# Performance work log

Hardware: AMD Instinct MI355X
Metric: run time of the kernel (lower is better)

The kernel has to match this reference:

```python
import jax, jax.numpy as jnp
import numpy as np

B, T, C = 4, 4096, 1024
HEAD = 128


def setup_inputs() -> dict:
    key = jax.random.key(0)
    k0, k1, k2, k3 = jax.random.split(key, 4)
    x = jax.random.normal(k0, (B, T, C), dtype=jnp.float32)
    # bias-free linear weights, stored as (in, out) so y = x @ W
    Wk = jax.random.normal(k1, (C, HEAD), dtype=jnp.float32) * (C ** -0.5)
    Wq = jax.random.normal(k2, (C, HEAD), dtype=jnp.float32) * (C ** -0.5)
    Wv = jax.random.normal(k3, (C, HEAD), dtype=jnp.float32) * (C ** -0.5)
    return {"x": x, "Wk": Wk, "Wq": Wq, "Wv": Wv}


def reference(x, Wk, Wq, Wv):
    Bx, Tx, Cx = x.shape
    k = x @ Wk            # [B,T,H]
    q = x @ Wq            # [B,T,H]
    v = x @ Wv            # [B,T,H]
    # NOTE: original code scales by C**-0.5 where C = n_embd (input dim), not head_size
    scale = Cx ** -0.5
    wei = jnp.einsum("bqh,bkh->bqk", q, k) * scale        # [B,T,T]
    causal = jnp.arange(Tx)[:, None] >= jnp.arange(Tx)[None, :]
    wei = jnp.where(causal, wei, -jnp.inf)
    wei = jax.nn.softmax(wei, axis=-1)
    # dropout rate is 0.0 in the source -> identity
    return jnp.einsum("bqk,bkh->bqh", wei, v)             # [B,T,H]
```

## Files before the change

kernel.cpp:

```cpp
#include <hip/hip_runtime.h>


typedef __bf16 bf16;
typedef bf16 bf16x8 __attribute__((ext_vector_type(8)));
typedef bf16 bf16x4 __attribute__((ext_vector_type(4)));
typedef float f32x4 __attribute__((ext_vector_type(4)));

#define L2E 1.4426950408889634f
#define TSEQ 4096
#define CDIM 1024
#define HDIM 128
#define MROWS 16384

#define GLDS(g, l)                                              \
  __builtin_amdgcn_global_load_lds(                             \
      (__attribute__((address_space(1))) void*)(g),             \
      (__attribute__((address_space(3))) void*)(l), 16, 0, 0)

static __device__ inline unsigned pkbf(float a, float b) {
  union { bf16 h; unsigned short u; } ua, ub;
  ua.h = (bf16)a; ub.h = (bf16)b;
  return ((unsigned)ub.u << 16) | (unsigned)ua.u;
}

__global__ __launch_bounds__(256) void wt_prep(const float* __restrict__ Wq,
                                               const float* __restrict__ Wk,
                                               const float* __restrict__ Wv,
                                               bf16* __restrict__ WT) {
  const int mode = blockIdx.y;
  const float* W = (mode == 0) ? Wq : (mode == 1) ? Wk : Wv;
  const int idx = blockIdx.x * 256 + threadIdx.x;
  const int n = idx >> 10;
  const int k = idx & 1023;
  WT[(size_t)mode * 131072 + idx] = (bf16)W[(size_t)k * HDIM + n];
}

__global__ __launch_bounds__(256) void qkv_gemm(const float* __restrict__ x,
                                                const bf16* __restrict__ WT,
                                                bf16* __restrict__ qb,
                                                bf16* __restrict__ kb,
                                                bf16* __restrict__ vT) {
  __shared__ __attribute__((aligned(16))) bf16 a_tile[128 * 32];
  __shared__ __attribute__((aligned(16))) bf16 b_tile[128 * 32];
  const int tid = threadIdx.x;
  const int wid = tid >> 6;
  const int lane = tid & 63;
  const int lr = lane & 15;
  const int lg = lane >> 4;
  const int wr = wid >> 1;
  const int wc = wid & 1;
  const int mode = blockIdx.y;
  const int m0 = blockIdx.x * 128;
  const bf16* wt = WT + (size_t)mode * 131072;

  int rowA[2], col8[2];
#pragma unroll
  for (int g = 0; g < 2; ++g) {
    const int idx8 = g * 256 + tid;
    rowA[g] = idx8 >> 2;
    col8[g] = (idx8 & 3) * 8;
  }

  f32x4 acc[4][4] = {};

  float4 fA[2][2];
  bf16x8 fB[2];
#pragma unroll
  for (int g = 0; g < 2; ++g) {
    const float* src = x + (size_t)(m0 + rowA[g]) * CDIM + col8[g];
    fA[g][0] = *(const float4*)src;
    fA[g][1] = *(const float4*)(src + 4);
    fB[g] = *(const bf16x8*)(wt + (size_t)rowA[g] * CDIM + col8[g]);
  }

#pragma unroll 1
  for (int kt = 0; kt < 32; ++kt) {
    __syncthreads();
#pragma unroll
    for (int g = 0; g < 2; ++g) {
      bf16x8 av;
      av[0] = (bf16)fA[g][0].x; av[1] = (bf16)fA[g][0].y;
      av[2] = (bf16)fA[g][0].z; av[3] = (bf16)fA[g][0].w;
      av[4] = (bf16)fA[g][1].x; av[5] = (bf16)fA[g][1].y;
      av[6] = (bf16)fA[g][1].z; av[7] = (bf16)fA[g][1].w;
      *(bf16x8*)&a_tile[rowA[g] * 32 + col8[g]] = av;
      *(bf16x8*)&b_tile[rowA[g] * 32 + col8[g]] = fB[g];
    }
    __syncthreads();
    if (kt + 1 < 32) {
#pragma unroll
      for (int g = 0; g < 2; ++g) {
        const float* src = x + (size_t)(m0 + rowA[g]) * CDIM + (kt + 1) * 32 + col8[g];
        fA[g][0] = *(const float4*)src;
        fA[g][1] = *(const float4*)(src + 4);
        fB[g] = *(const bf16x8*)(wt + (size_t)rowA[g] * CDIM + (kt + 1) * 32 + col8[g]);
      }
    }
    bf16x8 af[4], bfr[4];
#pragma unroll
    for (int r = 0; r < 4; ++r)
      af[r] = *(const bf16x8*)&a_tile[(wr * 64 + r * 16 + lr) * 32 + lg * 8];
#pragma unroll
    for (int c = 0; c < 4; ++c)
      bfr[c] = *(const bf16x8*)&b_tile[(wc * 64 + c * 16 + lr) * 32 + lg * 8];
#pragma unroll
    for (int r = 0; r < 4; ++r)
#pragma unroll
      for (int c = 0; c < 4; ++c)
        acc[r][c] = __builtin_amdgcn_mfma_f32_16x16x32_bf16(af[r], bfr[c], acc[r][c], 0, 0, 0);
  }

  if (mode < 2) {
    bf16* dst = (mode == 0) ? qb : kb;
    const float sc = (mode == 0) ? 0.03125f : 1.0f;
#pragma unroll
    for (int r = 0; r < 4; ++r)
#pragma unroll
      for (int c = 0; c < 4; ++c)
#pragma unroll
        for (int j = 0; j < 4; ++j) {
          const int row = m0 + wr * 64 + r * 16 + lg * 4 + j;
          const int col = wc * 64 + c * 16 + lr;
          dst[(size_t)row * HDIM + col] = (bf16)(acc[r][c][j] * sc);
        }
  } else {
#pragma unroll
    for (int r = 0; r < 4; ++r)
#pragma unroll
      for (int c = 0; c < 4; ++c) {
        const int row0 = m0 + wr * 64 + r * 16 + lg * 4;
        const int col = wc * 64 + c * 16 + lr;
        bf16x4 pv;
        pv[0] = (bf16)acc[r][c][0]; pv[1] = (bf16)acc[r][c][1];
        pv[2] = (bf16)acc[r][c][2]; pv[3] = (bf16)acc[r][c][3];
        *(bf16x4*)(vT + (size_t)col * MROWS + row0) = pv;
      }
  }
}

__global__ __launch_bounds__(256) void attn_part(const bf16* __restrict__ qb,
                                                 const bf16* __restrict__ kb,
                                                 const bf16* __restrict__ vT,
                                                 bf16* __restrict__ po,
                                                 float* __restrict__ pm,
                                                 float* __restrict__ pl,
                                                 int cshift, int maxc) {
  __shared__ __attribute__((aligned(16))) char kv_lds[2][32768];
  __shared__ __attribute__((aligned(16))) bf16 p_lds[4][16][72];
  const int tid = threadIdx.x;
  const int wid = tid >> 6;
  const int lane = tid & 63;
  const int lr = lane & 15;
  const int lg = lane >> 4;
  const int b = blockIdx.z;
  const int c = blockIdx.y;
  const int qbase = blockIdx.x * 64;
  const int kv0 = c << cshift;
  if (kv0 >= qbase + 64) return;
  const int kvend = min(kv0 + (1 << cshift), qbase + 64);
  const int nt = (kvend - kv0) >> 6;
  const int qr0 = qbase + wid * 16;
  const int grp = blockIdx.x * 4 + wid;
  const size_t qrow = (size_t)b * TSEQ + qr0;

  const int wbase = wid * 4096;
  int ksrc[4], vsrc[4];
#pragma unroll
  for (int i = 0; i < 4; ++i) {
    const int o = wbase + i * 1024 + lane * 16;
    const int rk = o >> 8;
    ksrc[i] = rk * 256 + ((o & 255) ^ ((rk & 7) << 4));
    const int rv = o >> 7;
    vsrc[i] = rv * (MROWS * 2) + ((o & 127) ^ ((rv & 7) << 4));
  }
  const char* kgb = (const char*)kb + (size_t)b * TSEQ * 256;
  const char* vgb = (const char*)vT + (size_t)b * TSEQ * 2;

  const int m30 = (lr & 3) << 4;
  const int m6 = (lr & 4) << 4;
  const int lgx = (lg * 16) ^ m30;
  const int kreadA = lr * 256 + lgx + m6;
  const int kreadB = lr * 256 + lgx + (64 ^ m6);
  const int vreadA = 16384 + lr * 128 + lgx + m6;
  const int vreadB = 16384 + lr * 128 + lgx + (64 ^ m6);

  bf16x8 qf[4];
#pragma unroll
  for (int d = 0; d < 4; ++d)
    qf[d] = *(const bf16x8*)(qb + (qrow + lr) * HDIM + d * 32 + lg * 8);

  f32x4 o_[8] = {};
  float m_ = -1e30f, l_ = 0.0f;

  {
    const char* ks = kgb + (size_t)kv0 * 256;
    const char* vs = vgb + (size_t)kv0 * 2;
#pragma unroll
    for (int i = 0; i < 4; ++i) {
      GLDS(ks + ksrc[i], &kv_lds[0][wbase + i * 1024]);
      GLDS(vs + vsrc[i], &kv_lds[0][16384 + wbase + i * 1024]);
    }
  }
  __syncthreads();

  int cur = 0;
  for (int t = 0; t < nt; ++t) {
    const int kvt = kv0 + (t << 6);
    if (t + 1 < nt) {
      const char* ks = kgb + (size_t)(kvt + 64) * 256;
      const char* vs = vgb + (size_t)(kvt + 64) * 2;
#pragma unroll
      for (int i = 0; i < 4; ++i) {
        GLDS(ks + ksrc[i], &kv_lds[cur ^ 1][wbase + i * 1024]);
        GLDS(vs + vsrc[i], &kv_lds[cur ^ 1][16384 + wbase + i * 1024]);
      }
    }
    if (kvt < qr0 + 16) {
      const char* kbuf = kv_lds[cur];
      f32x4 s[4] = {};
      __builtin_amdgcn_s_setprio(1);
#pragma unroll
      for (int nf = 0; nf < 4; ++nf) {
        const char* kb0 = kbuf + nf * 4096;
        bf16x8 kf;
        kf = *(const bf16x8*)(kb0 + kreadA);
        s[nf] = __builtin_amdgcn_mfma_f32_16x16x32_bf16(kf, qf[0], s[nf], 0, 0, 0);
        kf = *(const bf16x8*)(kb0 + kreadB);
        s[nf] = __builtin_amdgcn_mfma_f32_16x16x32_bf16(kf, qf[1], s[nf], 0, 0, 0);
        kf = *(const bf16x8*)(kb0 + kreadA + 128);
        s[nf] = __builtin_amdgcn_mfma_f32_16x16x32_bf16(kf, qf[2], s[nf], 0, 0, 0);
        kf = *(const bf16x8*)(kb0 + kreadB + 128);
        s[nf] = __builtin_amdgcn_mfma_f32_16x16x32_bf16(kf, qf[3], s[nf], 0, 0, 0);
      }
      __builtin_amdgcn_s_setprio(0);
      if (kvt + 63 >= qr0) {
        const int q = qr0 + lr;
#pragma unroll
        for (int nf = 0; nf < 4; ++nf)
#pragma unroll
          for (int j = 0; j < 4; ++j)
            if (kvt + nf * 16 + lg * 4 + j > q) s[nf][j] = -1e30f;
      }
      float rmax = fmaxf(fmaxf(s[0][0], s[0][1]), fmaxf(s[0][2], s[0][3]));
#pragma unroll
      for (int nf = 1; nf < 4; ++nf)
        rmax = fmaxf(rmax, fmaxf(fmaxf(s[nf][0], s[nf][1]), fmaxf(s[nf][2], s[nf][3])));
      rmax = fmaxf(rmax, __shfl_xor(rmax, 16));
      rmax = fmaxf(rmax, __shfl_xor(rmax, 32));
      const float mn = fmaxf(m_, rmax);
      const float al = exp2f((m_ - mn) * L2E);
      m_ = mn;
      float rsum = 0.0f;
#pragma unroll
      for (int nf = 0; nf < 4; ++nf)
#pragma unroll
        for (int j = 0; j < 4; ++j) {
          s[nf][j] = exp2f((s[nf][j] - mn) * L2E);
          rsum += s[nf][j];
        }
      rsum += __shfl_xor(rsum, 16);
      rsum += __shfl_xor(rsum, 32);
      l_ = l_ * al + rsum;
#pragma unroll
      for (int o = 0; o < 8; ++o)
#pragma unroll
        for (int j = 0; j < 4; ++j)
          o_[o][j] *= al;
      {
        unsigned* pw = (unsigned*)&p_lds[wid][0][0];
        const int base = lr * 36 + lg * 2;
#pragma unroll
        for (int nf = 0; nf < 4; ++nf) {
          pw[base + nf * 8]     = pkbf(s[nf][0], s[nf][1]);
          pw[base + nf * 8 + 1] = pkbf(s[nf][2], s[nf][3]);
        }
      }
      asm volatile("s_waitcnt lgkmcnt(0)" ::: "memory");
      __builtin_amdgcn_sched_barrier(0);
      bf16x8 pf0 = *(const bf16x8*)&p_lds[wid][lr][lg * 8];
      bf16x8 pf1 = *(const bf16x8*)&p_lds[wid][lr][32 + lg * 8];
      __builtin_amdgcn_s_setprio(1);
#pragma unroll
      for (int o = 0; o < 8; ++o) {
        bf16x8 vf;
        vf = *(const bf16x8*)(kbuf + vreadA + o * 2048);
        o_[o] = __builtin_amdgcn_mfma_f32_16x16x32_bf16(vf, pf0, o_[o], 0, 0, 0);
        vf = *(const bf16x8*)(kbuf + vreadB + o * 2048);
        o_[o] = __builtin_amdgcn_mfma_f32_16x16x32_bf16(vf, pf1, o_[o], 0, 0, 0);
      }
      __builtin_amdgcn_s_setprio(0);
    }
    __syncthreads();
    cur ^= 1;
  }

  const size_t slot = (size_t)(b * 256 + grp) * maxc + c;
  bf16* pob = po + slot * (16 * HDIM);
#pragma unroll
  for (int o = 0; o < 8; ++o) {
    bf16x4 pv;
    pv[0] = (bf16)o_[o][0]; pv[1] = (bf16)o_[o][1];
    pv[2] = (bf16)o_[o][2]; pv[3] = (bf16)o_[o][3];
    *(bf16x4*)(pob + lr * HDIM + o * 16 + lg * 4) = pv;
  }
  if (lg == 0) {
    pm[slot * 16 + lr] = m_;
    pl[slot * 16 + lr] = l_;
  }
}

__global__ __launch_bounds__(256) void attn_merge(const bf16* __restrict__ po,
                                                  const float* __restrict__ pm,
                                                  const float* __restrict__ pl,
                                                  float* __restrict__ out,
                                                  int cshift, int maxc) {
  const int bg = blockIdx.x;
  const int g = bg & 255;
  const int nch = ((g << 4) >> cshift) + 1;
  const int row = threadIdx.x >> 4;
  const int d8 = (threadIdx.x & 15) * 8;
  const size_t slot0 = (size_t)bg * maxc;

  float M = -1e30f;
  for (int c = 0; c < nch; ++c) M = fmaxf(M, pm[(slot0 + c) * 16 + row]);
  float L = 0.0f;
  float acc[8] = {};
  for (int c = 0; c < nch; ++c) {
    const float w = exp2f((pm[(slot0 + c) * 16 + row] - M) * L2E);
    L += w * pl[(slot0 + c) * 16 + row];
    const bf16x8 v = *(const bf16x8*)(po + (slot0 + c) * (16 * HDIM) + row * HDIM + d8);
#pragma unroll
    for (int i = 0; i < 8; ++i) acc[i] += w * (float)v[i];
  }
  const float inv = 1.0f / L;
  f32x4 r0, r1;
#pragma unroll
  for (int i = 0; i < 4; ++i) { r0[i] = acc[i] * inv; r1[i] = acc[i + 4] * inv; }
  float* dst = out + (size_t)bg * (16 * HDIM) + row * HDIM + d8;
  *(f32x4*)dst = r0;
  *(f32x4*)(dst + 4) = r1;
}

extern "C" void kernel_launch(void* const* d_in, const int* in_sizes, int n_in,
                              void* d_out, int out_size, void* d_ws, size_t ws_size,
                              hipStream_t stream) {
  const float* x  = (const float*)d_in[0];
  const float* Wk = (const float*)d_in[1];
  const float* Wq = (const float*)d_in[2];
  const float* Wv = (const float*)d_in[3];
  float* out = (float*)d_out;

  char* ws = (char*)d_ws;
  bf16* qb = (bf16*)(ws);
  bf16* kb = (bf16*)(ws + 4194304);
  bf16* vT = (bf16*)(ws + 8388608);
  bf16* WT = (bf16*)(ws + 12582912);
  const size_t pbase = 13369344;

  int cshift, maxc;
  if (ws_size >= pbase + 8ull * 1024 * 4224) { cshift = 9;  maxc = 8; }
  else if (ws_size >= pbase + 4ull * 1024 * 4224) { cshift = 10; maxc = 4; }
  else { cshift = 12; maxc = 1; }
  bf16* po = (bf16*)(ws + pbase);
  float* pm = (float*)(ws + pbase + (size_t)maxc * 1024 * 16 * 128 * 2);
  float* pl = pm + (size_t)maxc * 1024 * 16;

  wt_prep<<<dim3(512, 3), 256, 0, stream>>>(Wq, Wk, Wv, WT);
  qkv_gemm<<<dim3(128, 3), 256, 0, stream>>>(x, WT, qb, kb, vT);
  attn_part<<<dim3(64, maxc, 4), 256, 0, stream>>>(qb, kb, vT, po, pm, pl, cshift, maxc);
  attn_merge<<<1024, 256, 0, stream>>>(po, pm, pl, out, cshift, maxc);
}
```

Measured before the change: 103.6 us.

## Process 32 query rows per wave and skip small max rescales in attention

After: 101.5 us. 2.0% less time.

```diff
diff --git a/kernel.cpp b/kernel.cpp
--- a/kernel.cpp
+++ b/kernel.cpp
@@ -138,15 +138,15 @@
   }
 }
 
-__global__ __launch_bounds__(256) void attn_part(const bf16* __restrict__ qb,
-                                                 const bf16* __restrict__ kb,
-                                                 const bf16* __restrict__ vT,
-                                                 bf16* __restrict__ po,
-                                                 float* __restrict__ pm,
-                                                 float* __restrict__ pl,
-                                                 int cshift, int maxc) {
+__global__ __launch_bounds__(256, 2) void attn_part(const bf16* __restrict__ qg,
+                                                    const bf16* __restrict__ kb,
+                                                    const bf16* __restrict__ vT,
+                                                    bf16* __restrict__ po,
+                                                    float* __restrict__ pm,
+                                                    float* __restrict__ pl,
+                                                    int cshift, int maxc) {
   __shared__ __attribute__((aligned(16))) char kv_lds[2][32768];
-  __shared__ __attribute__((aligned(16))) bf16 p_lds[4][16][72];
+  __shared__ __attribute__((aligned(16))) bf16 p_lds[4][32][64];
   const int tid = threadIdx.x;
   const int wid = tid >> 6;
   const int lane = tid & 63;
@@ -154,14 +154,14 @@
   const int lg = lane >> 4;
   const int b = blockIdx.z;
   const int c = blockIdx.y;
-  const int qbase = blockIdx.x * 64;
+  const int qbase = blockIdx.x * 128;
   const int kv0 = c << cshift;
-  if (kv0 >= qbase + 64) return;
-  const int kvend = min(kv0 + (1 << cshift), qbase + 64);
+  if (kv0 >= qbase + 128) return;
+  const int kvend = min(kv0 + (1 << cshift), qbase + 128);
   const int nt = (kvend - kv0) >> 6;
-  const int qr0 = qbase + wid * 16;
-  const int grp = blockIdx.x * 4 + wid;
-  const size_t qrow = (size_t)b * TSEQ + qr0;
+  const int qr0w = qbase + wid * 32;
+  const int grp0 = blockIdx.x * 8 + wid * 2;
+  const size_t qrow = (size_t)b * TSEQ + qr0w;
 
   const int wbase = wid * 4096;
   int ksrc[4], vsrc[4];
@@ -176,6 +176,7 @@
   const char* kgb = (const char*)kb + (size_t)b * TSEQ * 256;
   const char* vgb = (const char*)vT + (size_t)b * TSEQ * 2;
 
+  const int msk = (lr & 7) << 4;
   const int m30 = (lr & 3) << 4;
   const int m6 = (lr & 4) << 4;
   const int lgx = (lg * 16) ^ m30;
@@ -184,13 +185,16 @@
   const int vreadA = 16384 + lr * 128 + lgx + m6;
   const int vreadB = 16384 + lr * 128 + lgx + (64 ^ m6);
 
-  bf16x8 qf[4];
-#pragma unroll
-  for (int d = 0; d < 4; ++d)
-    qf[d] = *(const bf16x8*)(qb + (qrow + lr) * HDIM + d * 32 + lg * 8);
-
-  f32x4 o_[8] = {};
-  float m_ = -1e30f, l_ = 0.0f;
+  bf16x8 qa[4], qc[4];
+#pragma unroll
+  for (int d = 0; d < 4; ++d) {
+    qa[d] = *(const bf16x8*)(qg + (qrow + lr) * HDIM + d * 32 + lg * 8);
+    qc[d] = *(const bf16x8*)(qg + (qrow + 16 + lr) * HDIM + d * 32 + lg * 8);
+  }
+
+  f32x4 o0_[8] = {}, o1_[8] = {};
+  float m0_ = -1e30f, l0_ = 0.0f;
+  float m1_ = -1e30f, l1_ = 0.0f;
 
   {
     const char* ks = kgb + (size_t)kv0 * 256;
@@ -215,78 +219,98 @@
         GLDS(vs + vsrc[i], &kv_lds[cur ^ 1][16384 + wbase + i * 1024]);
       }
     }
-    if (kvt < qr0 + 16) {
+    if (kvt < qr0w + 32) {
       const char* kbuf = kv_lds[cur];
-      f32x4 s[4] = {};
+      f32x4 s0[4] = {}, s1[4] = {};
       __builtin_amdgcn_s_setprio(1);
 #pragma unroll
       for (int nf = 0; nf < 4; ++nf) {
         const char* kb0 = kbuf + nf * 4096;
         bf16x8 kf;
         kf = *(const bf16x8*)(kb0 + kreadA);
-        s[nf] = __builtin_amdgcn_mfma_f32_16x16x32_bf16(kf, qf[0], s[nf], 0, 0, 0);
+        s0[nf] = __builtin_amdgcn_mfma_f32_16x16x32_bf16(kf, qa[0], s0[nf], 0, 0, 0);
+        s1[nf] = __builtin_amdgcn_mfma_f32_16x16x32_bf16(kf, qc[0], s1[nf], 0, 0, 0);
         kf = *(const bf16x8*)(kb0 + kreadB);
-        s[nf] = __builtin_amdgcn_mfma_f32_16x16x32_bf16(kf, qf[1], s[nf], 0, 0, 0);
+        s0[nf] = __builtin_amdgcn_mfma_f32_16x16x32_bf16(kf, qa[1], s0[nf], 0, 0, 0);
+        s1[nf] = __builtin_amdgcn_mfma_f32_16x16x32_bf16(kf, qc[1], s1[nf], 0, 0, 0);
         kf = *(const bf16x8*)(kb0 + kreadA + 128);
-        s[nf] = __builtin_amdgcn_mfma_f32_16x16x32_bf16(kf, qf[2], s[nf], 0, 0, 0);
+        s0[nf] = __builtin_amdgcn_mfma_f32_16x16x32_bf16(kf, qa[2], s0[nf], 0, 0, 0);
+        s1[nf] = __builtin_amdgcn_mfma_f32_16x16x32_bf16(kf, qc[2], s1[nf], 0, 0, 0);
         kf = *(const bf16x8*)(kb0 + kreadB + 128);
-        s[nf] = __builtin_amdgcn_mfma_f32_16x16x32_bf16(kf, qf[3], s[nf], 0, 0, 0);
+        s0[nf] = __builtin_amdgcn_mfma_f32_16x16x32_bf16(kf, qa[3], s0[nf], 0, 0, 0);
+        s1[nf] = __builtin_amdgcn_mfma_f32_16x16x32_bf16(kf, qc[3], s1[nf], 0, 0, 0);
       }
       __builtin_amdgcn_s_setprio(0);
-      if (kvt + 63 >= qr0) {
-        const int q = qr0 + lr;
+      if (kvt + 63 >= qr0w) {
+        const int q0 = qr0w + lr;
+        const int q1 = q0 + 16;
 #pragma unroll
         for (int nf = 0; nf < 4; ++nf)
 #pragma unroll
-          for (int j = 0; j < 4; ++j)
-            if (kvt + nf * 16 + lg * 4 + j > q) s[nf][j] = -1e30f;
-      }
-      float rmax = fmaxf(fmaxf(s[0][0], s[0][1]), fmaxf(s[0][2], s[0][3]));
-#pragma unroll
-      for (int nf = 1; nf < 4; ++nf)
-        rmax = fmaxf(rmax, fmaxf(fmaxf(s[nf][0], s[nf][1]), fmaxf(s[nf][2], s[nf][3])));
-      rmax = fmaxf(rmax, __shfl_xor(rmax, 16));
-      rmax = fmaxf(rmax, __shfl_xor(rmax, 32));
-      const float mn = fmaxf(m_, rmax);
-      const float al = exp2f((m_ - mn) * L2E);
-      m_ = mn;
-      float rsum = 0.0f;
+          for (int j = 0; j < 4; ++j) {
+            const int key = kvt + nf * 16 + lg * 4 + j;
+            if (key > q0) s0[nf][j] = -1e30f;
+            if (key > q1) s1[nf][j] = -1e30f;
+          }
+      }
+      float r0 = fmaxf(fmaxf(s0[0][0], s0[0][1]), fmaxf(s0[0][2], s0[0][3]));
+      float r1 = fmaxf(fmaxf(s1[0][0], s1[0][1]), fmaxf(s1[0][2], s1[0][3]));
+#pragma unroll
+      for (int nf = 1; nf < 4; ++nf) {
+        r0 = fmaxf(r0, fmaxf(fmaxf(s0[nf][0], s0[nf][1]), fmaxf(s0[nf][2], s0[nf][3])));
+        r1 = fmaxf(r1, fmaxf(fmaxf(s1[nf][0], s1[nf][1]), fmaxf(s1[nf][2], s1[nf][3])));
+      }
+      r0 = fmaxf(r0, __shfl_xor(r0, 16)); r0 = fmaxf(r0, __shfl_xor(r0, 32));
+      r1 = fmaxf(r1, __shfl_xor(r1, 16)); r1 = fmaxf(r1, __shfl_xor(r1, 32));
+      if (!__all(r0 <= m0_ + 8.0f && r1 <= m1_ + 8.0f)) {
+        const float mn0 = fmaxf(m0_, r0), mn1 = fmaxf(m1_, r1);
+        const float al0 = exp2f((m0_ - mn0) * L2E);
+        const float al1 = exp2f((m1_ - mn1) * L2E);
+        m0_ = mn0; m1_ = mn1;
+        l0_ *= al0; l1_ *= al1;
+#pragma unroll
+        for (int o = 0; o < 8; ++o)
+#pragma unroll
+          for (int j = 0; j < 4; ++j) { o0_[o][j] *= al0; o1_[o][j] *= al1; }
+      }
+      float rs0 = 0.0f, rs1 = 0.0f;
 #pragma unroll
       for (int nf = 0; nf < 4; ++nf)
 #pragma unroll
         for (int j = 0; j < 4; ++j) {
-          s[nf][j] = exp2f((s[nf][j] - mn) * L2E);
-          rsum += s[nf][j];
+          s0[nf][j] = exp2f((s0[nf][j] - m0_) * L2E); rs0 += s0[nf][j];
+          s1[nf][j] = exp2f((s1[nf][j] - m1_) * L2E); rs1 += s1[nf][j];
         }
-      rsum += __shfl_xor(rsum, 16);
-      rsum += __shfl_xor(rsum, 32);
-      l_ = l_ * al + rsum;
-#pragma unroll
-      for (int o = 0; o < 8; ++o)
-#pragma unroll
-        for (int j = 0; j < 4; ++j)
-          o_[o][j] *= al;
       {
-        unsigned* pw = (unsigned*)&p_lds[wid][0][0];
-        const int base = lr * 36 + lg * 2;
+        char* pw = (char*)p_lds + wid * 4096 + lr * 128;
 #pragma unroll
         for (int nf = 0; nf < 4; ++nf) {
-          pw[base + nf * 8]     = pkbf(s[nf][0], s[nf][1]);
-          pw[base + nf * 8 + 1] = pkbf(s[nf][2], s[nf][3]);
+          uint2 w2;
+          w2.x = pkbf(s0[nf][0], s0[nf][1]); w2.y = pkbf(s0[nf][2], s0[nf][3]);
+          *(uint2*)(pw + (((nf * 32) + lg * 8) ^ msk)) = w2;
+          w2.x = pkbf(s1[nf][0], s1[nf][1]); w2.y = pkbf(s1[nf][2], s1[nf][3]);
+          *(uint2*)(pw + 2048 + (((nf * 32) + lg * 8) ^ msk)) = w2;
         }
       }
+      rs0 += __shfl_xor(rs0, 16); rs0 += __shfl_xor(rs0, 32); l0_ += rs0;
+      rs1 += __shfl_xor(rs1, 16); rs1 += __shfl_xor(rs1, 32); l1_ += rs1;
       asm volatile("s_waitcnt lgkmcnt(0)" ::: "memory");
       __builtin_amdgcn_sched_barrier(0);
-      bf16x8 pf0 = *(const bf16x8*)&p_lds[wid][lr][lg * 8];
-      bf16x8 pf1 = *(const bf16x8*)&p_lds[wid][lr][32 + lg * 8];
+      const char* pr = (const char*)p_lds + wid * 4096 + lr * 128;
+      bf16x8 p00 = *(const bf16x8*)(pr + lgx + m6);
+      bf16x8 p01 = *(const bf16x8*)(pr + lgx + (64 ^ m6));
+      bf16x8 p10 = *(const bf16x8*)(pr + 2048 + lgx + m6);
+      bf16x8 p11 = *(const bf16x8*)(pr + 2048 + lgx + (64 ^ m6));
       __builtin_amdgcn_s_setprio(1);
 #pragma unroll
       for (int o = 0; o < 8; ++o) {
         bf16x8 vf;
         vf = *(const bf16x8*)(kbuf + vreadA + o * 2048);
-        o_[o] = __builtin_amdgcn_mfma_f32_16x16x32_bf16(vf, pf0, o_[o], 0, 0, 0);
+        o0_[o] = __builtin_amdgcn_mfma_f32_16x16x32_bf16(vf, p00, o0_[o], 0, 0, 0);
+        o1_[o] = __builtin_amdgcn_mfma_f32_16x16x32_bf16(vf, p10, o1_[o], 0, 0, 0);
         vf = *(const bf16x8*)(kbuf + vreadB + o * 2048);
-        o_[o] = __builtin_amdgcn_mfma_f32_16x16x32_bf16(vf, pf1, o_[o], 0, 0, 0);
+        o0_[o] = __builtin_amdgcn_mfma_f32_16x16x32_bf16(vf, p01, o0_[o], 0, 0, 0);
+        o1_[o] = __builtin_amdgcn_mfma_f32_16x16x32_bf16(vf, p11, o1_[o], 0, 0, 0);
       }
       __builtin_amdgcn_s_setprio(0);
     }
@@ -294,18 +318,23 @@
     cur ^= 1;
   }
 
-  const size_t slot = (size_t)(b * 256 + grp) * maxc + c;
-  bf16* pob = po + slot * (16 * HDIM);
+  const size_t slot0 = (size_t)(b * 256 + grp0) * maxc + c;
+  const size_t slot1 = slot0 + maxc;
+  bf16* pob0 = po + slot0 * (16 * HDIM);
+  bf16* pob1 = po + slot1 * (16 * HDIM);
 #pragma unroll
   for (int o = 0; o < 8; ++o) {
     bf16x4 pv;
-    pv[0] = (bf16)o_[o][0]; pv[1] = (bf16)o_[o][1];
-    pv[2] = (bf16)o_[o][2]; pv[3] = (bf16)o_[o][3];
-    *(bf16x4*)(pob + lr * HDIM + o * 16 + lg * 4) = pv;
+    pv[0] = (bf16)o0_[o][0]; pv[1] = (bf16)o0_[o][1];
+    pv[2] = (bf16)o0_[o][2]; pv[3] = (bf16)o0_[o][3];
+    *(bf16x4*)(pob0 + lr * HDIM + o * 16 + lg * 4) = pv;
+    pv[0] = (bf16)o1_[o][0]; pv[1] = (bf16)o1_[o][1];
+    pv[2] = (bf16)o1_[o][2]; pv[3] = (bf16)o1_[o][3];
+    *(bf16x4*)(pob1 + lr * HDIM + o * 16 + lg * 4) = pv;
   }
   if (lg == 0) {
-    pm[slot * 16 + lr] = m_;
-    pl[slot * 16 + lr] = l_;
+    pm[slot0 * 16 + lr] = m0_; pl[slot0 * 16 + lr] = l0_;
+    pm[slot1 * 16 + lr] = m1_; pl[slot1 * 16 + lr] = l1_;
   }
 }
 
@@ -367,6 +396,6 @@
 
   wt_prep<<<dim3(512, 3), 256, 0, stream>>>(Wq, Wk, Wv, WT);
   qkv_gemm<<<dim3(128, 3), 256, 0, stream>>>(x, WT, qb, kb, vT);
-  attn_part<<<dim3(64, maxc, 4), 256, 0, stream>>>(qb, kb, vT, po, pm, pl, cshift, maxc);
+  attn_part<<<dim3(32, maxc, 4), 256, 0, stream>>>(qb, kb, vT, po, pm, pl, cshift, maxc);
   attn_merge<<<1024, 256, 0, stream>>>(po, pm, pl, out, cshift, maxc);
 }
```

## Widen attention blocks to 8 waves, add lazy rescale and swizzled P tile

Applied to the files above, without the earlier changes.

Result: faster. 100.7 us (-2.8%).

```diff
diff --git a/kernel.cpp b/kernel.cpp
--- a/kernel.cpp
+++ b/kernel.cpp
@@ -138,15 +138,15 @@
   }
 }
 
-__global__ __launch_bounds__(256) void attn_part(const bf16* __restrict__ qb,
-                                                 const bf16* __restrict__ kb,
-                                                 const bf16* __restrict__ vT,
-                                                 bf16* __restrict__ po,
-                                                 float* __restrict__ pm,
-                                                 float* __restrict__ pl,
-                                                 int cshift, int maxc) {
+__global__ __launch_bounds__(512, 4) void attn_part(const bf16* __restrict__ qg,
+                                                    const bf16* __restrict__ kb,
+                                                    const bf16* __restrict__ vT,
+                                                    bf16* __restrict__ po,
+                                                    float* __restrict__ pm,
+                                                    float* __restrict__ pl,
+                                                    int cshift, int maxc) {
   __shared__ __attribute__((aligned(16))) char kv_lds[2][32768];
-  __shared__ __attribute__((aligned(16))) bf16 p_lds[4][16][72];
+  __shared__ __attribute__((aligned(16))) bf16 p_lds[8][16][64];
   const int tid = threadIdx.x;
   const int wid = tid >> 6;
   const int lane = tid & 63;
@@ -154,19 +154,19 @@
   const int lg = lane >> 4;
   const int b = blockIdx.z;
   const int c = blockIdx.y;
-  const int qbase = blockIdx.x * 64;
+  const int qbase = blockIdx.x * 128;
   const int kv0 = c << cshift;
-  if (kv0 >= qbase + 64) return;
-  const int kvend = min(kv0 + (1 << cshift), qbase + 64);
+  if (kv0 >= qbase + 128) return;
+  const int kvend = min(kv0 + (1 << cshift), qbase + 128);
   const int nt = (kvend - kv0) >> 6;
   const int qr0 = qbase + wid * 16;
-  const int grp = blockIdx.x * 4 + wid;
+  const int grp = blockIdx.x * 8 + wid;
   const size_t qrow = (size_t)b * TSEQ + qr0;
 
-  const int wbase = wid * 4096;
-  int ksrc[4], vsrc[4];
-#pragma unroll
-  for (int i = 0; i < 4; ++i) {
+  const int wbase = wid * 2048;
+  int ksrc[2], vsrc[2];
+#pragma unroll
+  for (int i = 0; i < 2; ++i) {
     const int o = wbase + i * 1024 + lane * 16;
     const int rk = o >> 8;
     ksrc[i] = rk * 256 + ((o & 255) ^ ((rk & 7) << 4));
@@ -176,6 +176,7 @@
   const char* kgb = (const char*)kb + (size_t)b * TSEQ * 256;
   const char* vgb = (const char*)vT + (size_t)b * TSEQ * 2;
 
+  const int msk = (lr & 7) << 4;
   const int m30 = (lr & 3) << 4;
   const int m6 = (lr & 4) << 4;
   const int lgx = (lg * 16) ^ m30;
@@ -187,7 +188,7 @@
   bf16x8 qf[4];
 #pragma unroll
   for (int d = 0; d < 4; ++d)
-    qf[d] = *(const bf16x8*)(qb + (qrow + lr) * HDIM + d * 32 + lg * 8);
+    qf[d] = *(const bf16x8*)(qg + (qrow + lr) * HDIM + d * 32 + lg * 8);
 
   f32x4 o_[8] = {};
   float m_ = -1e30f, l_ = 0.0f;
@@ -196,7 +197,7 @@
     const char* ks = kgb + (size_t)kv0 * 256;
     const char* vs = vgb + (size_t)kv0 * 2;
 #pragma unroll
-    for (int i = 0; i < 4; ++i) {
+    for (int i = 0; i < 2; ++i) {
       GLDS(ks + ksrc[i], &kv_lds[0][wbase + i * 1024]);
       GLDS(vs + vsrc[i], &kv_lds[0][16384 + wbase + i * 1024]);
     }
@@ -210,7 +211,7 @@
       const char* ks = kgb + (size_t)(kvt + 64) * 256;
       const char* vs = vgb + (size_t)(kvt + 64) * 2;
 #pragma unroll
-      for (int i = 0; i < 4; ++i) {
+      for (int i = 0; i < 2; ++i) {
         GLDS(ks + ksrc[i], &kv_lds[cur ^ 1][wbase + i * 1024]);
         GLDS(vs + vsrc[i], &kv_lds[cur ^ 1][16384 + wbase + i * 1024]);
       }
@@ -247,38 +248,39 @@
         rmax = fmaxf(rmax, fmaxf(fmaxf(s[nf][0], s[nf][1]), fmaxf(s[nf][2], s[nf][3])));
       rmax = fmaxf(rmax, __shfl_xor(rmax, 16));
       rmax = fmaxf(rmax, __shfl_xor(rmax, 32));
-      const float mn = fmaxf(m_, rmax);
-      const float al = exp2f((m_ - mn) * L2E);
-      m_ = mn;
+      if (!__all(rmax <= m_ + 8.0f)) {
+        const float mn = fmaxf(m_, rmax);
+        const float al = exp2f((m_ - mn) * L2E);
+        m_ = mn;
+        l_ *= al;
+#pragma unroll
+        for (int o = 0; o < 8; ++o)
+#pragma unroll
+          for (int j = 0; j < 4; ++j) o_[o][j] *= al;
+      }
       float rsum = 0.0f;
 #pragma unroll
       for (int nf = 0; nf < 4; ++nf)
 #pragma unroll
         for (int j = 0; j < 4; ++j) {
-          s[nf][j] = exp2f((s[nf][j] - mn) * L2E);
+          s[nf][j] = exp2f((s[nf][j] - m_) * L2E);
           rsum += s[nf][j];
         }
-      rsum += __shfl_xor(rsum, 16);
-      rsum += __shfl_xor(rsum, 32);
-      l_ = l_ * al + rsum;
-#pragma unroll
-      for (int o = 0; o < 8; ++o)
-#pragma unroll
-        for (int j = 0; j < 4; ++j)
-          o_[o][j] *= al;
       {
-        unsigned* pw = (unsigned*)&p_lds[wid][0][0];
-        const int base = lr * 36 + lg * 2;
+        char* pw = (char*)p_lds + wid * 2048 + lr * 128;
 #pragma unroll
         for (int nf = 0; nf < 4; ++nf) {
-          pw[base + nf * 8]     = pkbf(s[nf][0], s[nf][1]);
-          pw[base + nf * 8 + 1] = pkbf(s[nf][2], s[nf][3]);
+          uint2 w2;
+          w2.x = pkbf(s[nf][0], s[nf][1]); w2.y = pkbf(s[nf][2], s[nf][3]);
+          *(uint2*)(pw + (((nf * 32) + lg * 8) ^ msk)) = w2;
         }
       }
+      rsum += __shfl_xor(rsum, 16); rsum += __shfl_xor(rsum, 32); l_ += rsum;
       asm volatile("s_waitcnt lgkmcnt(0)" ::: "memory");
       __builtin_amdgcn_sched_barrier(0);
-      bf16x8 pf0 = *(const bf16x8*)&p_lds[wid][lr][lg * 8];
-      bf16x8 pf1 = *(const bf16x8*)&p_lds[wid][lr][32 + lg * 8];
+      const char* pr = (const char*)p_lds + wid * 2048 + lr * 128;
+      bf16x8 pf0 = *(const bf16x8*)(pr + lgx + m6);
+      bf16x8 pf1 = *(const bf16x8*)(pr + lgx + (64 ^ m6));
       __builtin_amdgcn_s_setprio(1);
 #pragma unroll
       for (int o = 0; o < 8; ++o) {
@@ -367,6 +369,6 @@
 
   wt_prep<<<dim3(512, 3), 256, 0, stream>>>(Wq, Wk, Wv, WT);
   qkv_gemm<<<dim3(128, 3), 256, 0, stream>>>(x, WT, qb, kb, vT);
-  attn_part<<<dim3(64, maxc, 4), 256, 0, stream>>>(qb, kb, vT, po, pm, pl, cshift, maxc);
+  attn_part<<<dim3(32, maxc, 4), 512, 0, stream>>>(qb, kb, vT, po, pm, pl, cshift, maxc);
   attn_merge<<<1024, 256, 0, stream>>>(po, pm, pl, out, cshift, maxc);
 }
```
